# Kernel tuning notes

Hardware: AMD Instinct MI355X
Metric: run time of the kernel (lower is better)

## Reference

```python
import jax, jax.numpy as jnp
import numpy as np

N = 10000
E = 320000
NEG_SLOPE = 0.01  # torch nn.LeakyReLU default


def leaky_relu(x):
    return jnp.where(x >= 0, x, NEG_SLOPE * x)


def spmm(row, col, vals, dense):
    # sparse[N,N] @ dense[N,D] via gather + segment_sum over destination rows
    msgs = vals[:, None] * dense[col]          # [E, D]
    return jax.ops.segment_sum(msgs, row, num_segments=N)


def setup_inputs() -> dict:
    key = jax.random.key(0)
    ks = jax.random.split(key, 7)
    z = jax.random.normal(ks[0], (N, 64), dtype=jnp.float32)
    adj_row = jax.random.randint(ks[1], (E,), 0, N, dtype=jnp.int64)
    adj_col = jax.random.randint(ks[2], (E,), 0, N, dtype=jnp.int64)
    adj_vals = jax.random.uniform(ks[3], (E,), dtype=jnp.float32)
    # xavier_uniform: bound = sqrt(6/(fan_in+fan_out))
    def xavier(k, out_d, in_d):
        b = np.sqrt(6.0 / (in_d + out_d)).astype(np.float32)
        return jax.random.uniform(k, (out_d, in_d), minval=-b, maxval=b, dtype=jnp.float32)
    w1 = xavier(ks[4], 128, 64)
    w2 = xavier(ks[5], 256, 128)
    w3 = xavier(ks[6], 512, 256)
    return {"z": z, "adj_row": adj_row, "adj_col": adj_col, "adj_vals": adj_vals,
            "w1": w1, "w2": w2, "w3": w3, "active": 1}


def gnn_layer(x, w, row, col, vals, active):
    support = x @ w.T  # F.linear(features, weight)
    if active:
        support = leaky_relu(support)
    return spmm(row, col, vals, support)


def reference(z, adj_row, adj_col, adj_vals, w1, w2, w3, active):
    x = gnn_layer(z, w1, adj_row, adj_col, adj_vals, active)
    x = gnn_layer(x, w2, adj_row, adj_col, adj_vals, active)
    x_hat = gnn_layer(x, w3, adj_row, adj_col, adj_vals, active)
    adj_hat = jax.nn.sigmoid(x_hat @ x_hat.T)  # [N, N]
    return (x_hat, adj_hat)
```

## Files before the change

kernel.cpp:

```cpp
#include <hip/hip_runtime.h>
#include <hip/hip_bf16.h>

#define N_NODES 10000
#define N_EDGES 320000
#define PADM    10112
#define DOUT3   512

typedef __attribute__((ext_vector_type(4))) float f32x4;
typedef __attribute__((ext_vector_type(8))) short bf16x8;
typedef __attribute__((ext_vector_type(8))) _Float16 f16x8;
typedef __attribute__((ext_vector_type(4))) _Float16 half4;
typedef __attribute__((ext_vector_type(2))) _Float16 half2;

#define GLOAD_LDS16(g, l)                                                        \
  __builtin_amdgcn_global_load_lds(                                              \
      (const __attribute__((address_space(1))) unsigned*)(g),                    \
      (__attribute__((address_space(3))) unsigned*)(l), 16, 0, 0)

__device__ inline unsigned short f2bf(float f) {
  union { float f; unsigned u; } uf; uf.f = f;
  unsigned u = uf.u;
  unsigned r = (u + 0x7fffu + ((u >> 16) & 1u)) >> 16;
  return (unsigned short)r;
}

__global__ __launch_bounds__(256) void k_zero(int* p, int n) {
  int i = blockIdx.x * 256 + threadIdx.x;
  if (i < n) p[i] = 0;
}

__global__ __launch_bounds__(256) void k_detect(const unsigned* rowsU32, int* flag) {
  __shared__ int any;
  if (threadIdx.x == 0) any = 0;
  __syncthreads();
  if (rowsU32[2 * threadIdx.x + 1] != 0u) any = 1;
  __syncthreads();
  if (threadIdx.x == 0) *flag = (any == 0) ? 1 : 0;
}

__device__ inline int edge_at(const void* p, int i, int is64) {
  return is64 ? (int)((const long long*)p)[i] : ((const int*)p)[i];
}

__global__ __launch_bounds__(256) void k_hist(const void* rows, const int* flag, int* cnt) {
  int i = blockIdx.x * 256 + threadIdx.x;
  if (i >= N_EDGES) return;
  int is64 = *flag;
  atomicAdd(&cnt[edge_at(rows, i, is64)], 1);
}

__global__ __launch_bounds__(256) void k_scan(const int* __restrict__ cnt, int* __restrict__ rp) {
  __shared__ int partial[256];
  const int T = 256;
  int t = threadIdx.x;
  int chunk = (N_NODES + T - 1) / T;
  int start = t * chunk;
  int end = start + chunk; if (end > N_NODES) end = N_NODES;
  int s = 0;
  for (int i = start; i < end && i >= start; ++i) s += cnt[i];
  partial[t] = (start < N_NODES) ? s : 0;
  __syncthreads();
  if (t == 0) {
    int acc = 0;
    for (int i = 0; i < T; ++i) { int v = partial[i]; partial[i] = acc; acc += v; }
  }
  __syncthreads();
  int acc = partial[t];
  for (int i = start; i < end && i >= start; ++i) { rp[i] = acc; acc += cnt[i]; }
  if (t == T - 1) rp[N_NODES] = acc;
}

__global__ __launch_bounds__(256) void k_scatter(const void* rows, const void* cols,
    const float* __restrict__ vals, const int* __restrict__ flag,
    const int* __restrict__ rp, int* cnt2, int* __restrict__ ccol, float* __restrict__ cval) {
  int i = blockIdx.x * 256 + threadIdx.x;
  if (i >= N_EDGES) return;
  int is64 = *flag;
  int r = edge_at(rows, i, is64);
  int c = edge_at(cols, i, is64);
  int pos = rp[r] + atomicAdd(&cnt2[r], 1);
  ccol[pos] = c;
  cval[pos] = vals[i];
}

#define Z4   160000
#define W14  2048
#define W24  8192
#define W34  32768
__global__ __launch_bounds__(256) void k_f2h_all(const float* __restrict__ z, const float* __restrict__ w1,
    const float* __restrict__ w2, const float* __restrict__ w3,
    _Float16* __restrict__ zh, _Float16* __restrict__ w1h,
    _Float16* __restrict__ w2h, _Float16* __restrict__ w3h) {
  int t = blockIdx.x * 256 + threadIdx.x;
  const float* src; _Float16* dst; int idx;
  if (t < Z4)                        { src = z;  dst = zh;  idx = t; }
  else if (t < Z4 + W14)             { src = w1; dst = w1h; idx = t - Z4; }
  else if (t < Z4 + W14 + W24)       { src = w2; dst = w2h; idx = t - Z4 - W14; }
  else if (t < Z4 + W14 + W24 + W34) { src = w3; dst = w3h; idx = t - Z4 - W14 - W24; }
  else return;
  const float4 f = *(const float4*)(src + (size_t)idx * 4);
  half4 h;
  h[0] = (_Float16)f.x; h[1] = (_Float16)f.y; h[2] = (_Float16)f.z; h[3] = (_Float16)f.w;
  *(half4*)(dst + (size_t)idx * 4) = h;
}

template <int K>
__global__ __launch_bounds__(256) void k_linh(const _Float16* __restrict__ A,
    const _Float16* __restrict__ W, _Float16* __restrict__ outh,
    int M, int Dout, const int* __restrict__ activeFlag) {
  __shared__ __align__(16) unsigned short As[128 * 64];
  __shared__ __align__(16) unsigned short Bs[128 * 64];
  const int tid = threadIdx.x;
  const int m0 = blockIdx.x * 128, n0 = blockIdx.y * 128;
  const int wave = tid >> 6, lane = tid & 63;
  const int wm = (wave >> 1) << 6;
  const int wn = (wave & 1) << 6;
  const int lr = lane & 15;
  const int lko = (lane >> 4) << 3;

  const int lrow8 = lane >> 3;
  const int lcol  = (lane & 7) << 3;
  int arows[4]; const _Float16* gb[4];
  unsigned short *la[4], *lb[4];
#pragma unroll
  for (int j = 0; j < 4; ++j) {
    const int c = wave * 4 + j;
    int ar = m0 + c * 8 + lrow8; if (ar > M - 1) ar = M - 1;
    arows[j] = ar;
    gb[j] = W + (size_t)(n0 + c * 8 + lrow8) * K + lcol;
    la[j] = &As[c * 512];
    lb[j] = &Bs[c * 512];
  }

  f32x4 acc[4][4];
#pragma unroll
  for (int i = 0; i < 4; ++i)
#pragma unroll
    for (int j = 0; j < 4; ++j)
#pragma unroll
      for (int q = 0; q < 4; ++q) acc[i][j][q] = 0.f;

  for (int k0 = 0; k0 < K; k0 += 64) {
    __syncthreads();
#pragma unroll
    for (int j = 0; j < 4; ++j) {
      GLOAD_LDS16(A + (size_t)arows[j] * K + k0 + lcol, la[j]);
      GLOAD_LDS16(gb[j] + k0, lb[j]);
    }
    __syncthreads();

#pragma unroll
    for (int kk = 0; kk < 64; kk += 32) {
      f16x8 af[4], bff[4];
#pragma unroll
      for (int f = 0; f < 4; ++f) {
        af[f]  = *(const f16x8*)&As[(wm + f * 16 + lr) * 64 + kk + lko];
        bff[f] = *(const f16x8*)&Bs[(wn + f * 16 + lr) * 64 + kk + lko];
      }
#pragma unroll
      for (int mi = 0; mi < 4; ++mi)
#pragma unroll
        for (int ni = 0; ni < 4; ++ni)
          acc[mi][ni] = __builtin_amdgcn_mfma_f32_16x16x32_f16(af[mi], bff[ni], acc[mi][ni], 0, 0, 0);
    }
  }

  const bool act = (*activeFlag) != 0;
#pragma unroll
  for (int mi = 0; mi < 4; ++mi) {
#pragma unroll
    for (int ni = 0; ni < 4; ++ni) {
      const int col = n0 + wn + ni * 16 + lr;
      const int rbase = m0 + wm + mi * 16 + ((lane >> 4) << 2);
#pragma unroll
      for (int q = 0; q < 4; ++q) {
        const int rr = rbase + q;
        if (rr < M) {
          float v = acc[mi][ni][q];
          if (act && v < 0.f) v *= 0.01f;
          outh[(size_t)rr * Dout + col] = (_Float16)v;
        }
      }
    }
  }
}

template <int D, int MODE>
__global__ __launch_bounds__(128) void k_spmmh(const int* __restrict__ rp,
    const int* __restrict__ ccol, const float* __restrict__ cval,
    const _Float16* __restrict__ sup, _Float16* __restrict__ outh,
    float* __restrict__ outf, unsigned short* __restrict__ outb) {
  constexpr int V = D / 128;
  const int r = blockIdx.x;
  const int d0 = threadIdx.x * V;
  const int s = rp[r], e = rp[r + 1];
  float acc[V];
#pragma unroll
  for (int v = 0; v < V; ++v) acc[v] = 0.f;

  for (int i = s; i < e; ++i) {
    const float w = cval[i];
    const _Float16* src = sup + (size_t)ccol[i] * D + d0;
    if constexpr (V == 4) {
      const half4 x = *(const half4*)src;
#pragma unroll
      for (int v = 0; v < 4; ++v) acc[v] = fmaf(w, (float)x[v], acc[v]);
    } else if constexpr (V == 2) {
      const half2 x = *(const half2*)src;
      acc[0] = fmaf(w, (float)x[0], acc[0]);
      acc[1] = fmaf(w, (float)x[1], acc[1]);
    } else {
      acc[0] = fmaf(w, (float)*src, acc[0]);
    }
  }

  if constexpr (MODE == 0) {
    if constexpr (V == 4) {
      half4 h; h[0] = (_Float16)acc[0]; h[1] = (_Float16)acc[1]; h[2] = (_Float16)acc[2]; h[3] = (_Float16)acc[3];
      *(half4*)(outh + (size_t)r * D + d0) = h;
    } else if constexpr (V == 2) {
      half2 h; h[0] = (_Float16)acc[0]; h[1] = (_Float16)acc[1];
      *(half2*)(outh + (size_t)r * D + d0) = h;
    } else {
      outh[(size_t)r * D + d0] = (_Float16)acc[0];
    }
  } else {
    *(float4*)(outf + (size_t)r * D + d0) = make_float4(acc[0], acc[1], acc[2], acc[3]);
    uint2 u;
    u.x = (unsigned)f2bf(acc[0]) | ((unsigned)f2bf(acc[1]) << 16);
    u.y = (unsigned)f2bf(acc[2]) | ((unsigned)f2bf(acc[3]) << 16);
    *(uint2*)(outb + (size_t)r * 512 + d0) = u;
  }
}

__global__ __launch_bounds__(256) void k_padzero(unsigned short* __restrict__ xb) {
  const int t = blockIdx.x * 256 + threadIdx.x;
  if (t >= (PADM - N_NODES) * 512 / 8) return;
  uint4 z; z.x = z.y = z.z = z.w = 0u;
  *(uint4*)&xb[(size_t)N_NODES * 512 + (size_t)t * 8] = z;
}

__global__ __launch_bounds__(256) void k_xxt2(const unsigned short* __restrict__ Xb,
                                              float* __restrict__ adj) {
  __shared__ __align__(16) unsigned short As[128 * 64];
  __shared__ __align__(16) unsigned short Bs[128 * 64];
  const int tid = threadIdx.x;
  const int m0 = blockIdx.x * 128, n0 = blockIdx.y * 128;
  const int wave = tid >> 6, lane = tid & 63;
  const int wm = (wave >> 1) << 6;
  const int wn = (wave & 1) << 6;
  const int lr = lane & 15;
  const int lko = (lane >> 4) << 3;

  const int lrow8 = lane >> 3;
  const int lcol  = (lane & 7) << 3;
  const unsigned short *gaA[4], *gaB[4];
  unsigned short *la[4], *lb[4];
#pragma unroll
  for (int j = 0; j < 4; ++j) {
    const int c = wave * 4 + j;
    gaA[j] = Xb + (size_t)(m0 + c * 8 + lrow8) * 512 + lcol;
    gaB[j] = Xb + (size_t)(n0 + c * 8 + lrow8) * 512 + lcol;
    la[j] = &As[c * 512];
    lb[j] = &Bs[c * 512];
  }

  f32x4 acc[4][4];
#pragma unroll
  for (int i = 0; i < 4; ++i)
#pragma unroll
    for (int j = 0; j < 4; ++j)
#pragma unroll
      for (int q = 0; q < 4; ++q) acc[i][j][q] = 0.f;

  for (int k0 = 0; k0 < 512; k0 += 64) {
    __syncthreads();
#pragma unroll
    for (int j = 0; j < 4; ++j) {
      GLOAD_LDS16(gaA[j] + k0, la[j]);
      GLOAD_LDS16(gaB[j] + k0, lb[j]);
    }
    __syncthreads();

#pragma unroll
    for (int kk = 0; kk < 64; kk += 32) {
      bf16x8 af[4], bff[4];
#pragma unroll
      for (int f = 0; f < 4; ++f) {
        af[f]  = *(const bf16x8*)&As[(wm + f * 16 + lr) * 64 + kk + lko];
        bff[f] = *(const bf16x8*)&Bs[(wn + f * 16 + lr) * 64 + kk + lko];
      }
#pragma unroll
      for (int mi = 0; mi < 4; ++mi)
#pragma unroll
        for (int ni = 0; ni < 4; ++ni)
          acc[mi][ni] = __builtin_amdgcn_mfma_f32_16x16x32_bf16(af[mi], bff[ni], acc[mi][ni], 0, 0, 0);
    }
  }

#pragma unroll
  for (int mi = 0; mi < 4; ++mi) {
#pragma unroll
    for (int ni = 0; ni < 4; ++ni) {
      const int col = n0 + wn + ni * 16 + lr;
      const int rbase = m0 + wm + mi * 16 + ((lane >> 4) << 2);
      if (col < N_NODES) {
#pragma unroll
        for (int q = 0; q < 4; ++q) {
          const int rr = rbase + q;
          if (rr < N_NODES) {
            const float s = acc[mi][ni][q];
            const float sg = __builtin_amdgcn_rcpf(1.0f + __expf(-s));
            __builtin_nontemporal_store(sg, &adj[(size_t)rr * N_NODES + col]);
          }
        }
      }
    }
  }
}

template <int K>
__global__ __launch_bounds__(256) void k_linear(const float* __restrict__ A,
    const float* __restrict__ W, float* __restrict__ C,
    int M, int Dout, const int* __restrict__ activeFlag) {
  __shared__ __align__(16) float As[16][68];
  __shared__ __align__(16) float Ws[16][68];
  const int m0 = blockIdx.x * 64;
  const int n0 = blockIdx.y * 64;
  const int tid = threadIdx.x;
  const int tx = tid & 15, ty = tid >> 4;
  const int lrow = tid >> 2;
  const int lk = (tid & 3) * 4;
  float acc[4][4];
#pragma unroll
  for (int i = 0; i < 4; ++i)
#pragma unroll
    for (int j = 0; j < 4; ++j) acc[i][j] = 0.f;

  for (int k0 = 0; k0 < K; k0 += 16) {
    float4 va = make_float4(0.f, 0.f, 0.f, 0.f);
    if (m0 + lrow < M) va = *(const float4*)(A + (size_t)(m0 + lrow) * K + k0 + lk);
    float4 vb = *(const float4*)(W + (size_t)(n0 + lrow) * K + k0 + lk);
    __syncthreads();
    As[lk + 0][lrow] = va.x; As[lk + 1][lrow] = va.y; As[lk + 2][lrow] = va.z; As[lk + 3][lrow] = va.w;
    Ws[lk + 0][lrow] = vb.x; Ws[lk + 1][lrow] = vb.y; Ws[lk + 2][lrow] = vb.z; Ws[lk + 3][lrow] = vb.w;
    __syncthreads();
#pragma unroll
    for (int kk = 0; kk < 16; ++kk) {
      const float4 a4 = *(const float4*)&As[kk][ty << 2];
      const float4 b4 = *(const float4*)&Ws[kk][tx << 2];
      const float av[4] = {a4.x, a4.y, a4.z, a4.w};
      const float bv[4] = {b4.x, b4.y, b4.z, b4.w};
#pragma unroll
      for (int i = 0; i < 4; ++i)
#pragma unroll
        for (int j = 0; j < 4; ++j) acc[i][j] = fmaf(av[i], bv[j], acc[i][j]);
    }
  }
  const bool act = (*activeFlag) != 0;
#pragma unroll
  for (int i = 0; i < 4; ++i) {
    const int row = m0 + (ty << 2) + i;
    if (row < M) {
#pragma unroll
      for (int j = 0; j < 4; ++j) {
        float v = acc[i][j];
        if (act && v < 0.f) v *= 0.01f;
        C[(size_t)row * Dout + n0 + (tx << 2) + j] = v;
      }
    }
  }
}

template <int D>
__global__ __launch_bounds__(128) void k_spmm2(const int* __restrict__ rp,
    const int* __restrict__ ccol, const float* __restrict__ cval,
    const float* __restrict__ sup, float* __restrict__ out) {
  constexpr int V = D / 128;
  const int r = blockIdx.x;
  const int d0 = threadIdx.x * V;
  const int s = rp[r], e = rp[r + 1];
  float acc[V];
#pragma unroll
  for (int v = 0; v < V; ++v) acc[v] = 0.f;
  for (int i = s; i < e; ++i) {
    const float w = cval[i];
    const float* src = sup + (size_t)ccol[i] * D + d0;
    if constexpr (V == 4) {
      const float4 x = *(const float4*)src;
      acc[0] = fmaf(w, x.x, acc[0]); acc[1] = fmaf(w, x.y, acc[1]);
      acc[2] = fmaf(w, x.z, acc[2]); acc[3] = fmaf(w, x.w, acc[3]);
    } else if constexpr (V == 2) {
      const float2 x = *(const float2*)src;
      acc[0] = fmaf(w, x.x, acc[0]); acc[1] = fmaf(w, x.y, acc[1]);
    } else {
      acc[0] = fmaf(w, *src, acc[0]);
    }
  }
  float* dst = out + (size_t)r * D + d0;
  if constexpr (V == 4) *(float4*)dst = make_float4(acc[0], acc[1], acc[2], acc[3]);
  else if constexpr (V == 2) *(float2*)dst = make_float2(acc[0], acc[1]);
  else *dst = acc[0];
}

__global__ __launch_bounds__(256) void k_xxt_f32(const float* __restrict__ Xf, float* __restrict__ adj) {
  __shared__ __align__(16) short As[128 * 32];
  __shared__ __align__(16) short Bs[128 * 32];
  const int tid = threadIdx.x;
  const int m0 = blockIdx.x * 128, n0 = blockIdx.y * 128;
  const int wave = tid >> 6, lane = tid & 63;
  const int wm = (wave >> 1) << 6;
  const int wn = (wave & 1) << 6;
  const int lr = lane & 15;
  const int lko = (lane >> 4) << 3;

  f32x4 acc[4][4];
#pragma unroll
  for (int i = 0; i < 4; ++i)
#pragma unroll
    for (int j = 0; j < 4; ++j)
#pragma unroll
      for (int q = 0; q < 4; ++q) acc[i][j][q] = 0.f;

  for (int k0 = 0; k0 < 512; k0 += 32) {
    __syncthreads();
#pragma unroll
    for (int h = 0; h < 2; ++h) {
      const int c = tid + h * 256;
      const int row = c >> 2;
      const int cq = (c & 3) << 3;
      float4 fa0 = make_float4(0, 0, 0, 0), fa1 = fa0, fb0 = fa0, fb1 = fa0;
      const int ga = m0 + row, gb = n0 + row;
      if (ga < N_NODES) {
        fa0 = *(const float4*)(Xf + (size_t)ga * 512 + k0 + cq);
        fa1 = *(const float4*)(Xf + (size_t)ga * 512 + k0 + cq + 4);
      }
      if (gb < N_NODES) {
        fb0 = *(const float4*)(Xf + (size_t)gb * 512 + k0 + cq);
        fb1 = *(const float4*)(Xf + (size_t)gb * 512 + k0 + cq + 4);
      }
      uint4 ua, ub;
      ua.x = (unsigned)f2bf(fa0.x) | ((unsigned)f2bf(fa0.y) << 16);
      ua.y = (unsigned)f2bf(fa0.z) | ((unsigned)f2bf(fa0.w) << 16);
      ua.z = (unsigned)f2bf(fa1.x) | ((unsigned)f2bf(fa1.y) << 16);
      ua.w = (unsigned)f2bf(fa1.z) | ((unsigned)f2bf(fa1.w) << 16);
      ub.x = (unsigned)f2bf(fb0.x) | ((unsigned)f2bf(fb0.y) << 16);
      ub.y = (unsigned)f2bf(fb0.z) | ((unsigned)f2bf(fb0.w) << 16);
      ub.z = (unsigned)f2bf(fb1.x) | ((unsigned)f2bf(fb1.y) << 16);
      ub.w = (unsigned)f2bf(fb1.z) | ((unsigned)f2bf(fb1.w) << 16);
      *(uint4*)&As[row * 32 + cq] = ua;
      *(uint4*)&Bs[row * 32 + cq] = ub;
    }
    __syncthreads();

    bf16x8 af[4], bff[4];
#pragma unroll
    for (int f = 0; f < 4; ++f) {
      af[f]  = *(const bf16x8*)&As[(wm + f * 16 + lr) * 32 + lko];
      bff[f] = *(const bf16x8*)&Bs[(wn + f * 16 + lr) * 32 + lko];
    }
#pragma unroll
    for (int mi = 0; mi < 4; ++mi)
#pragma unroll
      for (int ni = 0; ni < 4; ++ni)
        acc[mi][ni] = __builtin_amdgcn_mfma_f32_16x16x32_bf16(af[mi], bff[ni], acc[mi][ni], 0, 0, 0);
  }

#pragma unroll
  for (int mi = 0; mi < 4; ++mi) {
#pragma unroll
    for (int ni = 0; ni < 4; ++ni) {
      const int col = n0 + wn + ni * 16 + lr;
      const int rbase = m0 + wm + mi * 16 + ((lane >> 4) << 2);
      if (col < N_NODES) {
#pragma unroll
        for (int q = 0; q < 4; ++q) {
          const int rr = rbase + q;
          if (rr < N_NODES) {
            const float s = acc[mi][ni][q];
            adj[(size_t)rr * N_NODES + col] = 1.0f / (1.0f + __expf(-s));
          }
        }
      }
    }
  }
}

extern "C" void kernel_launch(void* const* d_in, const int* in_sizes, int n_in,
                              void* d_out, int out_size, void* d_ws, size_t ws_size,
                              hipStream_t stream) {
  const float* z     = (const float*)d_in[0];
  const void*  arow  = d_in[1];
  const void*  acol  = d_in[2];
  const float* avals = (const float*)d_in[3];
  const float* w1    = (const float*)d_in[4];
  const float* w2    = (const float*)d_in[5];
  const float* w3    = (const float*)d_in[6];
  const int*   activ = (const int*)d_in[7];

  float* out  = (float*)d_out;
  float* xhat = out;
  float* adj  = out + (size_t)N_NODES * DOUT3;

  int* iscr  = (int*)(adj + 9000000);
  int* rp    = iscr;
  int* cnt   = rp + 10016;
  int* cnt2  = cnt + 10016;
  int* flag  = cnt2 + 10016;
  int* ccol  = flag + 16;
  float* cval = (float*)(ccol + N_EDGES);

  _Float16* wsh = (_Float16*)d_ws;
  size_t off = 0;
  unsigned short* xb = (unsigned short*)d_ws;             off += (size_t)PADM * 512;
  _Float16* zh  = wsh + off;  off += 640000;
  _Float16* w1h = wsh + off;  off += 8192;
  _Float16* w2h = wsh + off;  off += 32768;
  _Float16* w3h = wsh + off;  off += 131072;
  _Float16* suph = wsh + off; off += (size_t)N_NODES * 512;
  _Float16* x1h = wsh + off;  off += (size_t)N_NODES * 128;
  _Float16* x2h = wsh + off;  off += (size_t)N_NODES * 256;
  const bool useWs = (ws_size >= off * sizeof(_Float16));

  k_zero<<<(20032 + 255) / 256, 256, 0, stream>>>(cnt, 20032);
  k_detect<<<1, 256, 0, stream>>>((const unsigned*)arow, flag);
  k_hist<<<(N_EDGES + 255) / 256, 256, 0, stream>>>(arow, flag, cnt);
  k_scan<<<1, 256, 0, stream>>>(cnt, rp);
  k_scatter<<<(N_EDGES + 255) / 256, 256, 0, stream>>>(arow, acol, avals, flag, rp, cnt2, ccol, cval);

  if (useWs) {
    k_f2h_all<<<(Z4 + W14 + W24 + W34 + 255) / 256, 256, 0, stream>>>(
        z, w1, w2, w3, zh, w1h, w2h, w3h);

    k_linh<64><<<dim3(79, 1), 256, 0, stream>>>(zh, w1h, suph, N_NODES, 128, activ);
    k_spmmh<128, 0><<<N_NODES, 128, 0, stream>>>(rp, ccol, cval, suph, x1h, nullptr, nullptr);
    k_linh<128><<<dim3(79, 2), 256, 0, stream>>>(x1h, w2h, suph, N_NODES, 256, activ);
    k_spmmh<256, 0><<<N_NODES, 128, 0, stream>>>(rp, ccol, cval, suph, x2h, nullptr, nullptr);
    k_linh<256><<<dim3(79, 4), 256, 0, stream>>>(x2h, w3h, suph, N_NODES, 512, activ);
    k_spmmh<512, 2><<<N_NODES, 128, 0, stream>>>(rp, ccol, cval, suph, nullptr, xhat, xb);

    k_padzero<<<28, 256, 0, stream>>>(xb);
    k_xxt2<<<dim3(79, 79), 256, 0, stream>>>(xb, adj);
  } else {
    float* sup = adj;
    float* x1  = adj + 5120000;
    float* x2  = x1 + 1280000;
    k_linear<64><<<dim3(157, 2), 256, 0, stream>>>(z, w1, sup, N_NODES, 128, activ);
    k_spmm2<128><<<N_NODES, 128, 0, stream>>>(rp, ccol, cval, sup, x1);
    k_linear<128><<<dim3(157, 4), 256, 0, stream>>>(x1, w2, sup, N_NODES, 256, activ);
    k_spmm2<256><<<N_NODES, 128, 0, stream>>>(rp, ccol, cval, sup, x2);
    k_linear<256><<<dim3(157, 8), 256, 0, stream>>>(x2, w3, sup, N_NODES, 512, activ);
    k_spmm2<512><<<N_NODES, 128, 0, stream>>>(rp, ccol, cval, sup, xhat);
    k_xxt_f32<<<dim3(79, 79), 256, 0, stream>>>(xhat, adj);
  }
}
```

Before: 779.8 us.

## Enlarge XX^T GEMM tile to 256x256 with 512 threads and block swizzle

New measurement: 776.2 us. Within noise of the previous version (-0.5%).

```diff
diff --git a/kernel.cpp b/kernel.cpp
--- a/kernel.cpp
+++ b/kernel.cpp
@@ -3,7 +3,7 @@
 
 #define N_NODES 10000
 #define N_EDGES 320000
-#define PADM    10112
+#define PADM    10240
 #define DOUT3   512
 
 typedef __attribute__((ext_vector_type(4))) float f32x4;
@@ -240,66 +240,66 @@
   *(uint4*)&xb[(size_t)N_NODES * 512 + (size_t)t * 8] = z;
 }
 
-__global__ __launch_bounds__(256) void k_xxt2(const unsigned short* __restrict__ Xb,
+__global__ __launch_bounds__(512) void k_xxt3(const unsigned short* __restrict__ Xb,
                                               float* __restrict__ adj) {
-  __shared__ __align__(16) unsigned short As[128 * 64];
-  __shared__ __align__(16) unsigned short Bs[128 * 64];
+  __shared__ __align__(16) unsigned short As[256 * 32];
+  __shared__ __align__(16) unsigned short Bs[256 * 32];
   const int tid = threadIdx.x;
-  const int m0 = blockIdx.x * 128, n0 = blockIdx.y * 128;
+
+  const int bid = blockIdx.x;
+  const int swz = (bid & 7) * 200 + (bid >> 3);
+  const int m0 = (swz % 40) * 256;
+  const int n0 = (swz / 40) * 256;
+
   const int wave = tid >> 6, lane = tid & 63;
-  const int wm = (wave >> 1) << 6;
-  const int wn = (wave & 1) << 6;
+  const int wm = (wave >> 2) << 7;
+  const int wn = (wave & 3) << 6;
   const int lr = lane & 15;
   const int lko = (lane >> 4) << 3;
 
-  const int lrow8 = lane >> 3;
-  const int lcol  = (lane & 7) << 3;
-  const unsigned short *gaA[4], *gaB[4];
-  unsigned short *la[4], *lb[4];
-#pragma unroll
-  for (int j = 0; j < 4; ++j) {
-    const int c = wave * 4 + j;
-    gaA[j] = Xb + (size_t)(m0 + c * 8 + lrow8) * 512 + lcol;
-    gaB[j] = Xb + (size_t)(n0 + c * 8 + lrow8) * 512 + lcol;
-    la[j] = &As[c * 512];
-    lb[j] = &Bs[c * 512];
-  }
-
-  f32x4 acc[4][4];
-#pragma unroll
-  for (int i = 0; i < 4; ++i)
+  const int c0 = wave * 2;
+  const int srow = c0 * 16 + (lane >> 2);
+  const int scol = (lane & 3) << 3;
+  const unsigned short* gA0 = Xb + (size_t)(m0 + srow) * 512 + scol;
+  const unsigned short* gA1 = gA0 + (size_t)16 * 512;
+  const unsigned short* gB0 = Xb + (size_t)(n0 + srow) * 512 + scol;
+  const unsigned short* gB1 = gB0 + (size_t)16 * 512;
+  unsigned short* lA0 = &As[c0 * 512];
+  unsigned short* lA1 = &As[(c0 + 1) * 512];
+  unsigned short* lB0 = &Bs[c0 * 512];
+  unsigned short* lB1 = &Bs[(c0 + 1) * 512];
+
+  f32x4 acc[8][4];
+#pragma unroll
+  for (int i = 0; i < 8; ++i)
 #pragma unroll
     for (int j = 0; j < 4; ++j)
 #pragma unroll
       for (int q = 0; q < 4; ++q) acc[i][j][q] = 0.f;
 
-  for (int k0 = 0; k0 < 512; k0 += 64) {
-    __syncthreads();
-#pragma unroll
-    for (int j = 0; j < 4; ++j) {
-      GLOAD_LDS16(gaA[j] + k0, la[j]);
-      GLOAD_LDS16(gaB[j] + k0, lb[j]);
-    }
-    __syncthreads();
-
-#pragma unroll
-    for (int kk = 0; kk < 64; kk += 32) {
-      bf16x8 af[4], bff[4];
-#pragma unroll
-      for (int f = 0; f < 4; ++f) {
-        af[f]  = *(const bf16x8*)&As[(wm + f * 16 + lr) * 64 + kk + lko];
-        bff[f] = *(const bf16x8*)&Bs[(wn + f * 16 + lr) * 64 + kk + lko];
-      }
-#pragma unroll
-      for (int mi = 0; mi < 4; ++mi)
-#pragma unroll
-        for (int ni = 0; ni < 4; ++ni)
-          acc[mi][ni] = __builtin_amdgcn_mfma_f32_16x16x32_bf16(af[mi], bff[ni], acc[mi][ni], 0, 0, 0);
-    }
-  }
-
-#pragma unroll
-  for (int mi = 0; mi < 4; ++mi) {
+  for (int k0 = 0; k0 < 512; k0 += 32) {
+    __syncthreads();
+    GLOAD_LDS16(gA0 + k0, lA0);
+    GLOAD_LDS16(gA1 + k0, lA1);
+    GLOAD_LDS16(gB0 + k0, lB0);
+    GLOAD_LDS16(gB1 + k0, lB1);
+    __syncthreads();
+
+    bf16x8 bf[4];
+#pragma unroll
+    for (int ni = 0; ni < 4; ++ni)
+      bf[ni] = *(const bf16x8*)&Bs[(wn + ni * 16 + lr) * 32 + lko];
+#pragma unroll
+    for (int mi = 0; mi < 8; ++mi) {
+      const bf16x8 am = *(const bf16x8*)&As[(wm + mi * 16 + lr) * 32 + lko];
+#pragma unroll
+      for (int ni = 0; ni < 4; ++ni)
+        acc[mi][ni] = __builtin_amdgcn_mfma_f32_16x16x32_bf16(am, bf[ni], acc[mi][ni], 0, 0, 0);
+    }
+  }
+
+#pragma unroll
+  for (int mi = 0; mi < 8; ++mi) {
 #pragma unroll
     for (int ni = 0; ni < 4; ++ni) {
       const int col = n0 + wn + ni * 16 + lr;
@@ -539,8 +539,8 @@
     k_linh<256><<<dim3(79, 4), 256, 0, stream>>>(x2h, w3h, suph, N_NODES, 512, activ);
     k_spmmh<512, 2><<<N_NODES, 128, 0, stream>>>(rp, ccol, cval, suph, nullptr, xhat, xb);
 
-    k_padzero<<<28, 256, 0, stream>>>(xb);
-    k_xxt2<<<dim3(79, 79), 256, 0, stream>>>(xb, adj);
+    k_padzero<<<60, 256, 0, stream>>>(xb);
+    k_xxt3<<<1600, 512, 0, stream>>>(xb, adj);
   } else {
     float* sup = adj;
     float* x1  = adj + 5120000;
```
